# Kernel optimization log

Measured on AMD Instinct MI355X. Metric: run time of the kernel, lower is better.

The kernel has to match this reference:

```python
import jax, jax.numpy as jnp
import numpy as np

B, T, D, R = 8, 4096, 512, 1024  # batch, tokens, dim, merges per sequence


def setup_inputs() -> dict:
    key = jax.random.key(0)
    k1, k2 = jax.random.split(key, 2)
    x = jax.random.normal(k1, (B, T, D), jnp.float32)
    W = jax.random.normal(k2, (D, D), jnp.float32) * (1.0 / np.sqrt(D))
    b = jnp.zeros((D,), jnp.float32)
    return {"x": x, "W": W, "b": b}


def _l2norm(v):
    # matches torch F.normalize(p=2, eps=1e-12)
    return v / jnp.maximum(jnp.linalg.norm(v, axis=-1, keepdims=True), 1e-12)


def _scatter_rows(arr, idx, vals):
    # arr: (B, T, d); idx: (B, r); vals: (B, r, d) -> set rows along axis 1
    Bn, _, d = arr.shape
    return arr.at[jnp.arange(Bn)[:, None, None], idx[:, :, None], jnp.arange(d)[None, None, :]].set(vals)


def _tome_forward(x, W, b, r):
    Bn, Tn, d = x.shape
    dst = x[:, 0::2, :]   # even positions
    src = x[:, 1::2, :]   # odd positions
    # cosine similarity bipartite scores: (B, T/2, T/2)
    scores = jnp.einsum('bsd,btd->bst', _l2norm(src), _l2norm(dst))
    best_scores = scores.max(axis=-1)          # (B, T_src)
    best_local = scores.argmax(axis=-1)        # (B, T_src)
    _, top_src = jax.lax.top_k(best_scores, r) # (B, r) src tokens with strongest match
    src_idx = top_src * 2 + 1                  # odd original positions
    dst_idx = jnp.take_along_axis(best_local, top_src, axis=1) * 2  # even original positions
    bidx = jnp.arange(Bn)[:, None]
    merged_away = jnp.zeros((Bn, Tn), bool).at[bidx, src_idx].set(True)

    # --- merge: average src into matched dst, drop src rows ---
    src_vals = jnp.take_along_axis(x, src_idx[:, :, None], axis=1)
    dst_vals = jnp.take_along_axis(x, dst_idx[:, :, None], axis=1)
    x_out = _scatter_rows(x, dst_idx, (src_vals + dst_vals) * 0.5)
    # kept positions in ascending order (stable sort: False before True)
    col = jnp.argsort(merged_away, axis=1, stable=True)[:, :Tn - r]  # (B, T-r)
    merged = jnp.take_along_axis(x_out, col[:, :, None], axis=1)     # (B, T-r, d)

    # --- wrapped dense layer ---
    hidden = merged @ W + b

    # --- unmerge: scatter kept rows back, copy dst value into src slots ---
    out = _scatter_rows(jnp.zeros((Bn, Tn, d), x.dtype), col, hidden)
    dvals = jnp.take_along_axis(out, dst_idx[:, :, None], axis=1)
    out = _scatter_rows(out, src_idx, dvals)
    return out


def reference(x, W, b):
    return _tome_forward(x, W, b, R)
```

## Files before the change

### kernel.cpp

```cpp
#include <hip/hip_runtime.h>
#include <stdint.h>

#define NB   8
#define TOK  4096
#define DIM  512
#define HALF 2048
#define RR   1024

typedef unsigned long long u64;
typedef unsigned int u32;
typedef _Float16 f16;
typedef f16 f16x4 __attribute__((ext_vector_type(4)));
typedef f16 f16x8 __attribute__((ext_vector_type(8)));
typedef float f32x4 __attribute__((ext_vector_type(4)));

#define AS1 __attribute__((address_space(1)))
#define AS3 __attribute__((address_space(3)))
#define GLL16(GP, LP) __builtin_amdgcn_global_load_lds((const AS1 u32*)(GP), (AS3 u32*)(LP), 16, 0, 0)

__device__ __forceinline__ u32 mono_f32(float f) {
    u32 u = __float_as_uint(f);
    return (u & 0x80000000u) ? ~u : (u | 0x80000000u);
}
__device__ __forceinline__ u64 umax64(u64 a, u64 b) { return a > b ? a : b; }

__global__ void k_pre(const float* __restrict__ x, f16* __restrict__ xh, f16* __restrict__ xl,
                      float* __restrict__ invn, const float* __restrict__ W,
                      f16* __restrict__ Wh, f16* __restrict__ Wl,
                      u64* __restrict__ best, u64* __restrict__ wkey) {
    __shared__ float tile[64][65];
    int bid = blockIdx.x, tid = threadIdx.x;
    if (bid < 8192) {
        int row  = bid * 4 + (tid >> 6);
        int lane = tid & 63;
        const float* p = x + (size_t)row * DIM + 4 * lane;
        float4 v0 = *(const float4*)p;
        float4 v1 = *(const float4*)(p + 256);
        float va[8] = {v0.x, v0.y, v0.z, v0.w, v1.x, v1.y, v1.z, v1.w};
        f16x4 h0, h1, l0, l1;
#pragma unroll
        for (int e = 0; e < 4; ++e) {
            f16 hh = (f16)va[e];     h0[e] = hh;  l0[e] = (f16)(va[e] - (float)hh);
            f16 hh1 = (f16)va[e+4];  h1[e] = hh1; l1[e] = (f16)(va[e+4] - (float)hh1);
        }
        size_t off = (size_t)row * DIM + 4 * lane;
        *(f16x4*)(xh + off)       = h0;
        *(f16x4*)(xh + off + 256) = h1;
        *(f16x4*)(xl + off)       = l0;
        *(f16x4*)(xl + off + 256) = l1;
        float ss = va[0]*va[0] + va[1]*va[1] + va[2]*va[2] + va[3]*va[3]
                 + va[4]*va[4] + va[5]*va[5] + va[6]*va[6] + va[7]*va[7];
#pragma unroll
        for (int m = 32; m; m >>= 1) ss += __shfl_xor(ss, m, 64);
        if (lane == 0) invn[row] = 1.0f / fmaxf(sqrtf(ss), 1e-12f);
    } else if (bid < 8256) {
        int wb = bid - 8192;
        int k0 = (wb >> 3) * 64, n0 = (wb & 7) * 64;
#pragma unroll
        for (int i = 0; i < 16; ++i) {
            int idx = tid + 256 * i;
            int r = idx >> 6, c = idx & 63;
            tile[r][c] = W[(size_t)(k0 + r) * DIM + n0 + c];
        }
        __syncthreads();
#pragma unroll
        for (int i = 0; i < 16; ++i) {
            int idx = tid + 256 * i;
            int n = idx >> 6, k = idx & 63;
            float v = tile[k][n];
            f16 h = (f16)v;
            Wh[(size_t)(n0 + n) * DIM + k0 + k] = h;
            Wl[(size_t)(n0 + n) * DIM + k0 + k] = (f16)(v - (float)h);
        }
    } else {
        int i = (bid - 8256) * 256 + tid;
        if (i < NB * HALF) { best[i] = 0ull; wkey[i] = ~0ull; }
    }
}


#define STAGE4(AP, BP, LB, COL) { \
  _Pragma("unroll") for (int r_ = 0; r_ < 4; ++r_) { \
    size_t d_ = (size_t)(256 * r_ + 64 * w) * 8; \
    GLL16((AP##h) + rowA[r_] + (COL), (LB) + d_); \
    GLL16((AP##l) + rowA[r_] + (COL), (LB) + 8192 + d_); \
    GLL16((BP##h) + rowB[r_] + (COL), (LB) + 16384 + d_); \
    GLL16((BP##l) + rowB[r_] + (COL), (LB) + 24576 + d_); \
  } }

#define COMPUTE_STEP(LB) { \
  const f16* Ah_ = (LB) + (wr * 64 + rm) * 64; \
  const f16* Bh_ = (LB) + 16384 + (wc * 64 + rm) * 64; \
  _Pragma("unroll") for (int kk = 0; kk < 2; ++kk) { \
    int ex = 8 * ((kk * 4 + cc) ^ rm7); \
    f16x8 ah[4], al[4], bh[4], bl[4]; \
    _Pragma("unroll") for (int f = 0; f < 4; ++f) { \
      ah[f] = *(const f16x8*)(Ah_ + f * 1024 + ex); \
      al[f] = *(const f16x8*)(Ah_ + 8192 + f * 1024 + ex); \
      bh[f] = *(const f16x8*)(Bh_ + f * 1024 + ex); \
      bl[f] = *(const f16x8*)(Bh_ + 8192 + f * 1024 + ex); \
    } \
    _Pragma("unroll") for (int i = 0; i < 4; ++i) \
      _Pragma("unroll") for (int j = 0; j < 4; ++j) { \
        acc[i][j] = __builtin_amdgcn_mfma_f32_16x16x32_f16(ah[i], bh[j], acc[i][j], 0, 0, 0); \
        acc[i][j] = __builtin_amdgcn_mfma_f32_16x16x32_f16(al[i], bh[j], acc[i][j], 0, 0, 0); \
        acc[i][j] = __builtin_amdgcn_mfma_f32_16x16x32_f16(ah[i], bl[j], acc[i][j], 0, 0, 0); \
      } \
  } }

__launch_bounds__(256)
__global__ void k_scores(const f16* __restrict__ xh, const f16* __restrict__ xl,
                         const float* __restrict__ invn, u64* __restrict__ best) {
    __shared__ __align__(16) f16 L[2][4][128][64];
    int bx = blockIdx.x;
    int b = bx >> 8, sb = (bx >> 4) & 15, tb = bx & 15;
    int tid = threadIdx.x, lane = tid & 63, w = tid >> 6, wr = w >> 1, wc = w & 1;
    int cc = lane >> 4, rm = lane & 15, rm7 = rm & 7;
    f16* L0 = &L[0][0][0][0];
    f16* L1 = &L[1][0][0][0];

    f32x4 acc[4][4];
#pragma unroll
    for (int i = 0; i < 4; ++i)
#pragma unroll
        for (int j = 0; j < 4; ++j) acc[i][j] = (f32x4){0.f, 0.f, 0.f, 0.f};

    size_t rowA[4], rowB[4];
#pragma unroll
    for (int r = 0; r < 4; ++r) {
        int g = tid + 256 * r;
        int m = g >> 3;
        int chunk = (g & 7) ^ (m & 7);
        rowA[r] = ((size_t)b * TOK + 2 * (sb * 128 + m) + 1) * DIM + 8 * chunk;
        rowB[r] = ((size_t)b * TOK + 2 * (tb * 128 + m)    ) * DIM + 8 * chunk;
    }

    STAGE4(x, x, L0, 0)
    __syncthreads();
#pragma unroll 1
    for (int ks = 0; ks < 8; ++ks) {
        f16* Lc = (ks & 1) ? L1 : L0;
        f16* Ln = (ks & 1) ? L0 : L1;
        if (ks < 7) { int coln = (ks + 1) << 6; STAGE4(x, x, Ln, coln) }
        COMPUTE_STEP(Lc)
        __syncthreads();
    }

    float invd[4];
#pragma unroll
    for (int j = 0; j < 4; ++j) {
        int t = tb * 128 + wc * 64 + j * 16 + rm;
        invd[j] = invn[(size_t)b * TOK + 2 * t];
    }
#pragma unroll
    for (int i = 0; i < 4; ++i) {
#pragma unroll
        for (int r = 0; r < 4; ++r) {
            int s = sb * 128 + wr * 64 + i * 16 + cc * 4 + r;
            float invs = invn[(size_t)b * TOK + 2 * s + 1];
            u64 key = 0;
#pragma unroll
            for (int j = 0; j < 4; ++j) {
                int t = tb * 128 + wc * 64 + j * 16 + rm;
                float sc = acc[i][j][r] * invs * invd[j];
                u64 k = ((u64)mono_f32(sc) << 32) | (u32)(2047 - t);
                key = umax64(key, k);
            }
#pragma unroll
            for (int m = 1; m < 16; m <<= 1) {
                u32 lo = (u32)key, hi = (u32)(key >> 32);
                lo = __shfl_xor(lo, m, 64);
                hi = __shfl_xor(hi, m, 64);
                key = umax64(key, ((u64)hi << 32) | lo);
            }
            if (rm == 0) atomicMax(&best[b * HALF + s], key);
        }
    }
}

__global__ void k_topk(const u64* __restrict__ best, u64* __restrict__ wkey,
                       u32* __restrict__ member, u32* __restrict__ dstmap) {
    __shared__ u32 smono[HALF];
    int b = blockIdx.x >> 4, sc = blockIdx.x & 15;
    int tid = threadIdx.x;
#pragma unroll
    for (int r = 0; r < 8; ++r) { int s = r * 256 + tid; smono[s] = (u32)(best[b * HALF + s] >> 32); }
    __syncthreads();
    int s = sc * 128 + (tid >> 1);
    u32 ms = smono[s];
    int t0 = (tid & 1) * 1024;
    int cnt = 0;
    for (int t = t0; t < t0 + 1024; ++t) {
        u32 mt = smono[t];
        cnt += ((mt > ms) || (mt == ms && t < s)) ? 1 : 0;
    }
    int oth = __shfl_xor(cnt, 1, 64);
    if ((tid & 1) == 0) {
        int rank = cnt + oth;
        u64 k = best[b * HALF + s];
        u32 d = 2047u - (u32)(k & 0xffffffffu);
        dstmap[b * HALF + s] = d;
        u32 mem = (rank < RR) ? 1u : 0u;
        member[b * HALF + s] = mem;
        if (mem) {
            u64 key = (k & 0xffffffff00000000ull) | (u32)(2047 - s);
            atomicMin(&wkey[b * HALF + d], key);
        }
    }
}

__global__ void k_merge2(const float* __restrict__ x, const u64* __restrict__ wkey,
                         f16* __restrict__ xh, f16* __restrict__ xl) {
    int idx = blockIdx.x;
    int b = idx >> 11, d = idx & (HALF - 1);
    u64 wk = wkey[b * HALF + d];
    if (wk == ~0ull) return;
    int s = 2047 - (int)(wk & 0xffffffffu);
    const float* xd = x + ((size_t)b * TOK + 2 * d) * DIM;
    const float* xs = x + ((size_t)b * TOK + 2 * s + 1) * DIM;
    int l0 = threadIdx.x * 8;
    f16x8 h, l;
#pragma unroll
    for (int e = 0; e < 8; ++e) {
        float v = (xd[l0 + e] + xs[l0 + e]) * 0.5f;
        f16 hh = (f16)v;
        h[e] = hh;
        l[e] = (f16)(v - (float)hh);
    }
    size_t off = ((size_t)b * TOK + 2 * d) * DIM + l0;
    *(f16x8*)(xh + off) = h;
    *(f16x8*)(xl + off) = l;
}

__launch_bounds__(256)
__global__ void k_out(const f16* __restrict__ xh, const f16* __restrict__ xl,
                      const f16* __restrict__ Wh, const f16* __restrict__ Wl,
                      const float* __restrict__ bias, const u32* __restrict__ member,
                      const u32* __restrict__ dstmap, float* __restrict__ out) {
    __shared__ __align__(16) f16 L[2][4][128][64];
    int bx = blockIdx.x;
    int im = bx >> 2, in = bx & 3;
    int tid = threadIdx.x, lane = tid & 63, w = tid >> 6, wr = w >> 1, wc = w & 1;
    int cc = lane >> 4, rm = lane & 15, rm7 = rm & 7;
    f16* L0 = &L[0][0][0][0];
    f16* L1 = &L[1][0][0][0];

    f32x4 acc[4][4];
#pragma unroll
    for (int i = 0; i < 4; ++i)
#pragma unroll
        for (int j = 0; j < 4; ++j) acc[i][j] = (f32x4){0.f, 0.f, 0.f, 0.f};

    size_t rowA[4], rowB[4];
#pragma unroll
    for (int r = 0; r < 4; ++r) {
        int g = tid + 256 * r;
        int m = g >> 3;
        int chunk = (g & 7) ^ (m & 7);
        int grow = im * 128 + m;
        int b_ = grow >> 12, tok = grow & (TOK - 1);
        if (tok & 1) {
            int s = tok >> 1;
            if (member[b_ * HALF + s]) tok = 2 * (int)dstmap[b_ * HALF + s];
        }
        rowA[r] = (((size_t)b_ << 12) + tok) * DIM + 8 * chunk;
        rowB[r] = (size_t)(in * 128 + m) * DIM + 8 * chunk;
    }

    STAGE4(x, W, L0, 0)
    __syncthreads();
#pragma unroll 1
    for (int ks = 0; ks < 8; ++ks) {
        f16* Lc = (ks & 1) ? L1 : L0;
        f16* Ln = (ks & 1) ? L0 : L1;
        if (ks < 7) { int coln = (ks + 1) << 6; STAGE4(x, W, Ln, coln) }
        COMPUTE_STEP(Lc)
        __syncthreads();
    }

    float bj[4];
#pragma unroll
    for (int j = 0; j < 4; ++j) bj[j] = bias[in * 128 + wc * 64 + j * 16 + rm];
#pragma unroll
    for (int i = 0; i < 4; ++i) {
#pragma unroll
        for (int r = 0; r < 4; ++r) {
            int gm = im * 128 + wr * 64 + i * 16 + cc * 4 + r;
#pragma unroll
            for (int j = 0; j < 4; ++j) {
                int n = in * 128 + wc * 64 + j * 16 + rm;
                out[(size_t)gm * DIM + n] = acc[i][j][r] + bj[j];
            }
        }
    }
}

extern "C" void kernel_launch(void* const* d_in, const int* in_sizes, int n_in,
                              void* d_out, int out_size, void* d_ws, size_t ws_size,
                              hipStream_t stream) {
    const float* x    = (const float*)d_in[0];
    const float* W    = (const float*)d_in[1];
    const float* bias = (const float*)d_in[2];
    float* out = (float*)d_out;

    char* ws = (char*)d_ws;
    f16*   xh     = (f16*)(ws);
    f16*   xl     = (f16*)(ws + (32u << 20));
    f16*   Wh     = (f16*)(ws + (64u << 20));
    f16*   Wl     = (f16*)(ws + (64u << 20) + (512u << 10));
    float* invn   = (float*)(ws + (65u << 20));
    u64*   best   = (u64*)(ws + (65u << 20) + (128u << 10));
    u64*   wkey   = (u64*)(ws + (65u << 20) + (256u << 10));
    u32*   dstmap = (u32*)(ws + (65u << 20) + (384u << 10));
    u32*   member = (u32*)(ws + (65u << 20) + (448u << 10));

    hipLaunchKernelGGL(k_pre,    dim3(8320),  dim3(256), 0, stream, x, xh, xl, invn, W, Wh, Wl, best, wkey);
    hipLaunchKernelGGL(k_scores, dim3(2048),  dim3(256), 0, stream, xh, xl, invn, best);
    hipLaunchKernelGGL(k_topk,   dim3(128),   dim3(256), 0, stream, best, wkey, member, dstmap);
    hipLaunchKernelGGL(k_merge2, dim3(16384), dim3(64),  0, stream, x, wkey, xh, xl);
    hipLaunchKernelGGL(k_out,    dim3(1024),  dim3(256), 0, stream, xh, xl, Wh, Wl, bias, member, dstmap, out);
}
```

Before: 390.0 us.

## Drop LDS double-buffering in GEMM kernels to fit two blocks per CU

Both tiled MFMA kernels (scores and output projection) move from a double-buffered 128 KB LDS tile to a single 64 KB buffer, and launch bounds now request two blocks per CU. The loop now loads a tile, synchronises, computes, and synchronises again, with no prefetch of the next tile. The aim is to hide load latency through a second resident block instead of in-block prefetching. The risk is that loads are exposed within each block and register pressure is capped for occupancy 2, which could cause spills.

```diff
diff --git a/kernel.cpp b/kernel.cpp
--- a/kernel.cpp
+++ b/kernel.cpp
@@ -108,16 +108,15 @@
       } \
   } }
 
-__launch_bounds__(256)
+__launch_bounds__(256, 2)
 __global__ void k_scores(const f16* __restrict__ xh, const f16* __restrict__ xl,
                          const float* __restrict__ invn, u64* __restrict__ best) {
-    __shared__ __align__(16) f16 L[2][4][128][64];
+    __shared__ __align__(16) f16 L[4][128][64];
     int bx = blockIdx.x;
     int b = bx >> 8, sb = (bx >> 4) & 15, tb = bx & 15;
     int tid = threadIdx.x, lane = tid & 63, w = tid >> 6, wr = w >> 1, wc = w & 1;
     int cc = lane >> 4, rm = lane & 15, rm7 = rm & 7;
-    f16* L0 = &L[0][0][0][0];
-    f16* L1 = &L[1][0][0][0];
+    f16* L0 = &L[0][0][0];
 
     f32x4 acc[4][4];
 #pragma unroll
@@ -135,14 +134,12 @@
         rowB[r] = ((size_t)b * TOK + 2 * (tb * 128 + m)    ) * DIM + 8 * chunk;
     }
 
-    STAGE4(x, x, L0, 0)
-    __syncthreads();
 #pragma unroll 1
     for (int ks = 0; ks < 8; ++ks) {
-        f16* Lc = (ks & 1) ? L1 : L0;
-        f16* Ln = (ks & 1) ? L0 : L1;
-        if (ks < 7) { int coln = (ks + 1) << 6; STAGE4(x, x, Ln, coln) }
-        COMPUTE_STEP(Lc)
+        int col0 = ks << 6;
+        STAGE4(x, x, L0, col0)
+        __syncthreads();
+        COMPUTE_STEP(L0)
         __syncthreads();
     }
 
@@ -232,18 +229,17 @@
     *(f16x8*)(xl + off) = l;
 }
 
-__launch_bounds__(256)
+__launch_bounds__(256, 2)
 __global__ void k_out(const f16* __restrict__ xh, const f16* __restrict__ xl,
                       const f16* __restrict__ Wh, const f16* __restrict__ Wl,
                       const float* __restrict__ bias, const u32* __restrict__ member,
                       const u32* __restrict__ dstmap, float* __restrict__ out) {
-    __shared__ __align__(16) f16 L[2][4][128][64];
+    __shared__ __align__(16) f16 L[4][128][64];
     int bx = blockIdx.x;
     int im = bx >> 2, in = bx & 3;
     int tid = threadIdx.x, lane = tid & 63, w = tid >> 6, wr = w >> 1, wc = w & 1;
     int cc = lane >> 4, rm = lane & 15, rm7 = rm & 7;
-    f16* L0 = &L[0][0][0][0];
-    f16* L1 = &L[1][0][0][0];
+    f16* L0 = &L[0][0][0];
 
     f32x4 acc[4][4];
 #pragma unroll
@@ -267,14 +263,12 @@
         rowB[r] = (size_t)(in * 128 + m) * DIM + 8 * chunk;
     }
 
-    STAGE4(x, W, L0, 0)
-    __syncthreads();
 #pragma unroll 1
     for (int ks = 0; ks < 8; ++ks) {
-        f16* Lc = (ks & 1) ? L1 : L0;
-        f16* Ln = (ks & 1) ? L0 : L1;
-        if (ks < 7) { int coln = (ks + 1) << 6; STAGE4(x, W, Ln, coln) }
-        COMPUTE_STEP(Lc)
+        int col0 = ks << 6;
+        STAGE4(x, W, L0, col0)
+        __syncthreads();
+        COMPUTE_STEP(L0)
         __syncthreads();
     }
 
```

After: 331.4 us. 1.18x faster.
